# Performance work log

Measured on AMD Instinct MI355X. Metric: run time of the kernel, lower is better.

## Reference

```python
import jax, jax.numpy as jnp
import numpy as np

N, C1, C2 = 1024, 384, 128
H, SQK, SV, PQK, PV, OUT = 12, 16, 16, 4, 8, 384
EPS = 1e-8
DOUT = H*SV + 3*H*PV + H*PV + H*C2  # 2112


def setup_inputs():
    key = jax.random.key(0)
    ks = jax.random.split(key, 10)
    inputs_1d = jax.random.normal(ks[0], (N, C1), jnp.float32)
    inputs_2d = jax.random.normal(ks[1], (N, N, C2), jnp.float32)
    mask = jnp.ones((N, 1), jnp.float32)
    # random valid rotations from unit quaternions
    quat = jax.random.normal(ks[2], (N, 4), jnp.float32)
    quat = quat / jnp.linalg.norm(quat, axis=-1, keepdims=True)
    w, x, y, z = quat[:, 0], quat[:, 1], quat[:, 2], quat[:, 3]
    rot = jnp.stack([
        jnp.stack([1 - 2*(y*y + z*z), 2*(x*y - w*z), 2*(x*z + w*y)], -1),
        jnp.stack([2*(x*y + w*z), 1 - 2*(x*x + z*z), 2*(y*z - w*x)], -1),
        jnp.stack([2*(x*z - w*y), 2*(y*z + w*x), 1 - 2*(x*x + y*y)], -1)], -2)
    trans = 10.0 * jax.random.normal(ks[3], (N, 3), jnp.float32)
    s1 = 1.0 / np.sqrt(C1)
    wq = jax.random.normal(ks[4], (C1, H*SQK), jnp.float32) * s1
    bq = jnp.zeros((H*SQK,), jnp.float32)
    wkv = jax.random.normal(ks[5], (C1, H*(SQK + SV)), jnp.float32) * s1
    bkv = jnp.zeros((H*(SQK + SV),), jnp.float32)
    wqp = jax.random.normal(ks[6], (C1, H*3*PQK), jnp.float32) * s1
    bqp = jnp.zeros((H*3*PQK,), jnp.float32)
    wkvp = jax.random.normal(ks[7], (C1, H*3*(PQK + PV)), jnp.float32) * s1
    bkvp = jnp.zeros((H*3*(PQK + PV),), jnp.float32)
    w2d = jax.random.normal(ks[8], (C2, H), jnp.float32) / np.sqrt(C2)
    b2d = jnp.zeros((H,), jnp.float32)
    tpw = jnp.full((H,), np.log(np.e - 1.0), jnp.float32)  # softplus(tpw)=1 at init
    wo = jax.random.normal(ks[9], (DOUT, OUT), jnp.float32) / np.sqrt(DOUT)
    bo = jnp.zeros((OUT,), jnp.float32)
    return dict(inputs_1d=inputs_1d, inputs_2d=inputs_2d, mask=mask, rot=rot, trans=trans,
                wq=wq, bq=bq, wkv=wkv, bkv=bkv, wqp=wqp, bqp=bqp, wkvp=wkvp, bkvp=bkvp,
                w2d=w2d, b2d=b2d, tpw=tpw, wo=wo, bo=bo)


def _ipa(inputs_1d, inputs_2d, mask, rot, trans, wq, bq, wkv, bkv, wqp, bqp,
         wkvp, bkvp, w2d, b2d, tpw, wo, bo):
    n = inputs_1d.shape[0]
    # scalar q/k/v
    q_scalar = (inputs_1d @ wq + bq).reshape(n, H, SQK)
    kv_scalar = (inputs_1d @ wkv + bkv).reshape(n, H, SQK + SV)
    k_scalar, v_scalar = kv_scalar[..., :SQK], kv_scalar[..., SQK:]
    # point q/k/v: local frame -> global frame, x_g = R x_l + t
    q_pl = (inputs_1d @ wqp + bqp).reshape(n, 3, H*PQK)
    q_pg = jnp.einsum('nac,nck->nak', rot, q_pl) + trans[:, :, None]
    q_pt = q_pg.reshape(n, 3, H, PQK).transpose(1, 2, 0, 3)        # (3,H,N,PQK)
    kv_pl = (inputs_1d @ wkvp + bkvp).reshape(n, 3, H*(PQK + PV))
    kv_pg = jnp.einsum('nac,nck->nak', rot, kv_pl) + trans[:, :, None]
    kv_pt = kv_pg.reshape(n, 3, H, PQK + PV).transpose(1, 2, 0, 3)  # (3,H,N,PQK+PV)
    k_pt, v_pt = kv_pt[..., :PQK], kv_pt[..., PQK:]
    # logit weights (3 logit terms)
    scalar_w = np.sqrt(1.0 / (3.0 * SQK))
    point_w = np.sqrt(1.0 / (3.0 * PQK * 9.0 / 2.0)) * jax.nn.softplus(tpw)  # (H,)
    # squared-distance term, expanded to avoid a (3,H,N,N,P) intermediate
    sq = jnp.sum(q_pt * q_pt, axis=(0, 3))                         # (H,N)
    sk = jnp.sum(k_pt * k_pt, axis=(0, 3))                         # (H,N)
    qk = jnp.einsum('chnp,chmp->hnm', q_pt, k_pt)
    dist2 = sq[:, :, None] + sk[:, None, :] - 2.0 * qk             # (H,N,N)
    attn_qk_point = -0.5 * point_w[:, None, None] * dist2
    attn_qk_scalar = jnp.einsum('nhs,mhs->hnm', scalar_w * q_scalar, k_scalar)
    att2d = jnp.transpose(inputs_2d @ w2d + b2d, (2, 0, 1))        # (H,N,N)
    logits = attn_qk_scalar + attn_qk_point + np.sqrt(1.0 / 3.0) * att2d
    mask_2d = mask * jnp.swapaxes(mask, -1, -2)                    # (N,N)
    logits = logits - 1e5 * (1.0 - mask_2d)
    attn = jax.nn.softmax(logits, axis=-1)                         # (H,N,N)
    # aggregate scalar, point and pair outputs with the same weights
    res_scalar = jnp.einsum('hnm,mhs->nhs', attn, v_scalar).reshape(n, H*SV)
    res_pg = jnp.einsum('hnm,chmp->cnhp', attn, v_pt).reshape(3, n, H*PV)
    res_pl = jnp.einsum('nca,cnk->ank', rot, res_pg - trans.T[:, :, None])  # R^T(g-t)
    pt_norm = jnp.sqrt(EPS + jnp.sum(res_pl * res_pl, axis=0))     # (N,H*PV)
    res_2d = jnp.einsum('hnm,nmc->nhc', attn, inputs_2d).reshape(n, H*C2)
    final = jnp.concatenate([res_scalar, res_pl[0], res_pl[1], res_pl[2], pt_norm, res_2d], axis=-1)
    return final @ wo + bo


def reference(inputs_1d, inputs_2d, mask, rot, trans, wq, bq, wkv, bkv, wqp, bqp,
              wkvp, bkvp, w2d, b2d, tpw, wo, bo):
    return _ipa(inputs_1d, inputs_2d, mask, rot, trans, wq, bq, wkv, bkv, wqp, bqp,
                wkvp, bkvp, w2d, b2d, tpw, wo, bo)
```

## Files before the change

### kernel.cpp

```cpp
#include <hip/hip_runtime.h>
#include <math.h>

#define NN_ 1024
#define DOUT_ 2112
#define NOUT_ 384

using bf16x8_t = __attribute__((ext_vector_type(8))) short;
using f32x4_t  = __attribute__((ext_vector_type(4))) float;

__global__ __launch_bounds__(256) void k_gemm1(
    const float* __restrict__ in1,
    const float* __restrict__ wq, const float* __restrict__ bq,
    const float* __restrict__ wkv, const float* __restrict__ bkv,
    const float* __restrict__ wqp, const float* __restrict__ bqp,
    const float* __restrict__ wkvp, const float* __restrict__ bkvp,
    float* __restrict__ yraw)
{
    __shared__ float a_l[64 * 36];
    __shared__ float b_l[32 * 68];
    const int t = threadIdx.x;
    const int m0 = blockIdx.x * 64, j0 = blockIdx.y * 64;
    const int tx = t & 15, ty = t >> 4;
    float acc[4][4] = {};
    for (int k0 = 0; k0 < 384; k0 += 32) {
        #pragma unroll
        for (int e = 0; e < 2; ++e) {
            int idx = t + 256 * e;
            int r = idx >> 3, c4 = (idx & 7) * 4;
            *(float4*)&a_l[r * 36 + c4] = *(const float4*)&in1[(size_t)(m0 + r) * 384 + k0 + c4];
        }
        #pragma unroll
        for (int e = 0; e < 2; ++e) {
            int idx = t + 256 * e;
            int r = idx >> 4, c4 = (idx & 15) * 4;
            int j = j0 + c4;
            const float* w; int ncol, jj;
            if (j < 192)      { w = wq;   ncol = 192; jj = j; }
            else if (j < 576) { w = wkv;  ncol = 384; jj = j - 192; }
            else if (j < 720) { w = wqp;  ncol = 144; jj = j - 576; }
            else              { w = wkvp; ncol = 432; jj = j - 720; }
            *(float4*)&b_l[r * 68 + c4] = *(const float4*)&w[(size_t)(k0 + r) * ncol + jj];
        }
        __syncthreads();
        #pragma unroll 8
        for (int k = 0; k < 32; ++k) {
            float4 bv = *(const float4*)&b_l[k * 68 + tx * 4];
            #pragma unroll
            for (int i = 0; i < 4; ++i) {
                float av = a_l[(ty * 4 + i) * 36 + k];
                acc[i][0] += av * bv.x; acc[i][1] += av * bv.y;
                acc[i][2] += av * bv.z; acc[i][3] += av * bv.w;
            }
        }
        __syncthreads();
    }
    int j = j0 + tx * 4;
    float4 bias;
    {
        const float* b; int jj;
        if (j < 192)      { b = bq;   jj = j; }
        else if (j < 576) { b = bkv;  jj = j - 192; }
        else if (j < 720) { b = bqp;  jj = j - 576; }
        else              { b = bkvp; jj = j - 720; }
        bias = *(const float4*)&b[jj];
    }
    #pragma unroll
    for (int i = 0; i < 4; ++i) {
        float4 o;
        o.x = acc[i][0] + bias.x; o.y = acc[i][1] + bias.y;
        o.z = acc[i][2] + bias.z; o.w = acc[i][3] + bias.w;
        *(float4*)&yraw[(size_t)(m0 + ty * 4 + i) * 1152 + j] = o;
    }
}

__global__ __launch_bounds__(256) void k_rot(
    const float* __restrict__ yraw, const float* __restrict__ rotm, const float* __restrict__ trans,
    float* __restrict__ qp_arr, float* __restrict__ kpackT4, float* __restrict__ vpack,
    float* __restrict__ sq_arr, float* __restrict__ skT)
{
    __shared__ float rt_l[4][12];
    const int t = threadIdx.x;
    const int n0 = blockIdx.x * 4;
    if (t < 48) {
        int n_ = t / 12, i = t % 12;
        rt_l[n_][i] = (i < 9) ? rotm[(n0 + n_) * 9 + i] : trans[(n0 + n_) * 3 + (i - 9)];
    }
    __syncthreads();
    const int n_ = t >> 6, l = t & 63;
    const int n = n0 + n_;
    const float* y = yraw + (size_t)n * 1152;
    const float* R = rt_l[n_];
    #pragma unroll
    for (int jj = 0; jj < 9; ++jj) {
        int o = l + 64 * jj;
        if (o < 144) {
            int a = o / 48, kk = o % 48;
            float v = R[9 + a] + R[a*3+0] * y[576 + kk] + R[a*3+1] * y[576 + 48 + kk] + R[a*3+2] * y[576 + 96 + kk];
            qp_arr[(size_t)n * 144 + o] = v;
        } else if (o < 288) {
            int o2 = o - 144;
            int a = o2 / 48, r2 = o2 % 48;
            int kk = (r2 >> 2) * 12 + (r2 & 3);
            float v = R[9 + a] + R[a*3+0] * y[720 + kk] + R[a*3+1] * y[720 + 144 + kk] + R[a*3+2] * y[720 + 288 + kk];
            int j = 192 + o2;
            kpackT4[(size_t)(j >> 2) * 4096 + 4 * n + (j & 3)] = v;
        } else {
            int o3 = o - 288;
            int a = o3 / 96, r2 = o3 % 96;
            int kk = (r2 >> 3) * 12 + 4 + (r2 & 7);
            float v = R[9 + a] + R[a*3+0] * y[720 + kk] + R[a*3+1] * y[720 + 144 + kk] + R[a*3+2] * y[720 + 288 + kk];
            vpack[(size_t)n * 480 + 192 + o3] = v;
        }
    }
    #pragma unroll
    for (int jj = 0; jj < 3; ++jj) {
        int o = l + 64 * jj;
        int h = o >> 4, r2 = o & 15;
        kpackT4[(size_t)(o >> 2) * 4096 + 4 * n + (o & 3)] = y[192 + h * 32 + r2];
        vpack[(size_t)n * 480 + o] = y[192 + h * 32 + 16 + r2];
    }
    if (l < 24) {
        int which = l / 12, h = l % 12;
        int base = (which == 0) ? 576 : 720;
        int stride = (which == 0) ? 48 : 144;
        float s = 0.f;
        #pragma unroll
        for (int a = 0; a < 3; ++a) {
            #pragma unroll
            for (int p = 0; p < 4; ++p) {
                int kk = (which == 0) ? (h * 4 + p) : (h * 12 + p);
                float v = R[9 + a] + R[a*3+0] * y[base + kk] + R[a*3+1] * y[base + stride + kk] + R[a*3+2] * y[base + 2 * stride + kk];
                s += v * v;
            }
        }
        if (which == 0) sq_arr[(size_t)n * 12 + h] = s;
        else            skT[(size_t)h * 1024 + n] = s;
    }
}

__global__ __launch_bounds__(256) void k_attn8(
    const float* __restrict__ x2d, const float* __restrict__ mask,
    const float* __restrict__ w2d, const float* __restrict__ b2d, const float* __restrict__ tpw,
    const float* __restrict__ yraw, const float* __restrict__ qp_arr,
    const float* __restrict__ kpackT4, const float* __restrict__ vpack,
    const float* __restrict__ sq_arr, const float* __restrict__ skT,
    const float* __restrict__ rotm, const float* __restrict__ trans,
    float* __restrict__ fin)
{
    __shared__ unsigned short x_lT[128][72];
    __shared__ unsigned short tlb[16][72];
    __shared__ unsigned short w2bT[16][132];
    __shared__ float at2_l[64][13];
    __shared__ float qs_l[192], qp_l[144];
    __shared__ float sq_l[12], pw_l[12], b2_l[12];
    __shared__ float rmax_l[12], rsum_l[16], alph_l[16];
    __shared__ float rt_l[12];
    __shared__ float pg_l[288];

    const int t = threadIdx.x;
    const int n = blockIdx.x;

    const int wv = t >> 6, ln = t & 63;
    const int mmS = ln & 15, oS = ln >> 4;
    const int m3 = t & 63, hg = t >> 6;
    const int rowB = (ln >> 4) * 4;
    const int jF = 2 * t;
    const int hF = (jF < 192) ? (jF >> 4) : (((jF - 192) % 96) >> 3);

    f32x4_t accM[2] = {{0.f, 0.f, 0.f, 0.f}, {0.f, 0.f, 0.f, 0.f}};
    float accF0 = 0.f, accF1 = 0.f;
    float4 xpf[8];

    for (int i = t; i < 2112; i += 256) {
        int h = i / 132, c = i % 132;
        unsigned short v = 0;
        if (h < 12 && c < 128) v = (unsigned short)((__float_as_uint(w2d[c * 12 + h]) + 0x8000u) >> 16);
        w2bT[h][c] = v;
    }
    if (t < 192) qs_l[t] = yraw[(size_t)n * 1152 + t];
    if (t < 144) qp_l[t] = qp_arr[(size_t)n * 144 + t];
    if (t < 12) {
        sq_l[t] = sq_arr[(size_t)n * 12 + t];
        pw_l[t] = 0.13608276348795434f * log1pf(__expf(tpw[t]));
        b2_l[t] = b2d[t];
        rmax_l[t] = -3.0e38f;
        rt_l[t] = (t < 9) ? rotm[n * 9 + t] : trans[n * 3 + (t - 9)];
    }
    if (t < 16) { rsum_l[t] = 0.f; alph_l[t] = 1.0f; }
    const float maskn = mask[n];

    {
        const float* xr = x2d + ((size_t)n * NN_ + wv * 16 + mmS) * 128 + oS * 8;
        #pragma unroll
        for (int kk = 0; kk < 4; ++kk) {
            xpf[2 * kk]     = *(const float4*)&xr[kk * 32];
            xpf[2 * kk + 1] = *(const float4*)&xr[kk * 32 + 4];
        }
    }
    __syncthreads();

    for (int mt = 0; mt < 16; ++mt) {
        const int m0 = mt * 64;
        {
            bf16x8_t afr[4];
            #pragma unroll
            for (int kk = 0; kk < 4; ++kk) {
                unsigned short e0 = (unsigned short)((__float_as_uint(xpf[2*kk].x)   + 0x8000u) >> 16);
                unsigned short e1 = (unsigned short)((__float_as_uint(xpf[2*kk].y)   + 0x8000u) >> 16);
                unsigned short e2 = (unsigned short)((__float_as_uint(xpf[2*kk].z)   + 0x8000u) >> 16);
                unsigned short e3 = (unsigned short)((__float_as_uint(xpf[2*kk].w)   + 0x8000u) >> 16);
                unsigned short e4 = (unsigned short)((__float_as_uint(xpf[2*kk+1].x) + 0x8000u) >> 16);
                unsigned short e5 = (unsigned short)((__float_as_uint(xpf[2*kk+1].y) + 0x8000u) >> 16);
                unsigned short e6 = (unsigned short)((__float_as_uint(xpf[2*kk+1].z) + 0x8000u) >> 16);
                unsigned short e7 = (unsigned short)((__float_as_uint(xpf[2*kk+1].w) + 0x8000u) >> 16);
                afr[kk][0] = (short)e0; afr[kk][1] = (short)e1; afr[kk][2] = (short)e2; afr[kk][3] = (short)e3;
                afr[kk][4] = (short)e4; afr[kk][5] = (short)e5; afr[kk][6] = (short)e6; afr[kk][7] = (short)e7;
                const int c0 = kk * 32 + oS * 8;
                const int m = wv * 16 + mmS;
                x_lT[c0 + 0][m] = e0; x_lT[c0 + 1][m] = e1;
                x_lT[c0 + 2][m] = e2; x_lT[c0 + 3][m] = e3;
                x_lT[c0 + 4][m] = e4; x_lT[c0 + 5][m] = e5;
                x_lT[c0 + 6][m] = e6; x_lT[c0 + 7][m] = e7;
            }
            f32x4_t aA = {0.f, 0.f, 0.f, 0.f};
            #pragma unroll
            for (int kk = 0; kk < 4; ++kk) {
                bf16x8_t bfW = *(const bf16x8_t*)&w2bT[ln & 15][kk * 32 + (ln >> 4) * 8];
                aA = __builtin_amdgcn_mfma_f32_16x16x32_bf16(afr[kk], bfW, aA, 0, 0, 0);
            }
            const int hC = ln & 15;
            if (hC < 12) {
                #pragma unroll
                for (int r = 0; r < 4; ++r)
                    at2_l[wv * 16 + (ln >> 4) * 4 + r][hC] = aA[r];
            }
        }
        __syncthreads();

        {
            int m1 = (mt + 1 == 16) ? 0 : (m0 + 64);
            const float* xr = x2d + ((size_t)n * NN_ + m1 + wv * 16 + mmS) * 128 + oS * 8;
            #pragma unroll
            for (int kk = 0; kk < 4; ++kk) {
                xpf[2 * kk]     = *(const float4*)&xr[kk * 32];
                xpf[2 * kk + 1] = *(const float4*)&xr[kk * 32 + 4];
            }
        }
        {
            const int mg = m0 + m3;
            const float* kb = kpackT4 + 4 * (size_t)mg;
            const float mko = 100000.0f * (1.0f - maskn * mask[mg]);
            #pragma unroll
            for (int e = 0; e < 3; ++e) {
                const int h = hg * 3 + e;
                float4 k0 = *(const float4*)&kb[(size_t)(h * 4 + 0) * 4096];
                float4 k1 = *(const float4*)&kb[(size_t)(h * 4 + 1) * 4096];
                float4 k2 = *(const float4*)&kb[(size_t)(h * 4 + 2) * 4096];
                float4 k3 = *(const float4*)&kb[(size_t)(h * 4 + 3) * 4096];
                float4 p0 = *(const float4*)&kb[(size_t)(48 + h) * 4096];
                float4 p1 = *(const float4*)&kb[(size_t)(60 + h) * 4096];
                float4 p2 = *(const float4*)&kb[(size_t)(72 + h) * 4096];
                float skm = skT[(size_t)h * 1024 + mg];
                const float4* qsn = (const float4*)&qs_l[h * 16];
                float dqs = qsn[0].x*k0.x + qsn[0].y*k0.y + qsn[0].z*k0.z + qsn[0].w*k0.w
                          + qsn[1].x*k1.x + qsn[1].y*k1.y + qsn[1].z*k1.z + qsn[1].w*k1.w
                          + qsn[2].x*k2.x + qsn[2].y*k2.y + qsn[2].z*k2.z + qsn[2].w*k2.w
                          + qsn[3].x*k3.x + qsn[3].y*k3.y + qsn[3].z*k3.z + qsn[3].w*k3.w;
                float4 qA = *(const float4*)&qp_l[h * 4];
                float4 qB = *(const float4*)&qp_l[48 + h * 4];
                float4 qC = *(const float4*)&qp_l[96 + h * 4];
                float qk = qA.x*p0.x + qA.y*p0.y + qA.z*p0.z + qA.w*p0.w
                         + qB.x*p1.x + qB.y*p1.y + qB.z*p1.z + qB.w*p1.w
                         + qC.x*p2.x + qC.y*p2.y + qC.z*p2.z + qC.w*p2.w;
                float pwh = pw_l[h];
                float lg = 0.14433756729740643f * dqs
                         + pwh * qk - 0.5f * pwh * (sq_l[h] + skm)
                         + 0.57735026918962576f * (at2_l[m3][h] + b2_l[h])
                         - mko;
                float tm = lg;
                tm = fmaxf(tm, __shfl_xor(tm, 1));
                tm = fmaxf(tm, __shfl_xor(tm, 2));
                tm = fmaxf(tm, __shfl_xor(tm, 4));
                tm = fmaxf(tm, __shfl_xor(tm, 8));
                tm = fmaxf(tm, __shfl_xor(tm, 16));
                tm = fmaxf(tm, __shfl_xor(tm, 32));
                float om = rmax_l[h];
                float nm = fmaxf(om, tm);
                float p = __expf(lg - nm);
                tlb[h][m3] = (unsigned short)((__float_as_uint(p) + 0x8000u) >> 16);
                float ps = p;
                ps += __shfl_xor(ps, 1);
                ps += __shfl_xor(ps, 2);
                ps += __shfl_xor(ps, 4);
                ps += __shfl_xor(ps, 8);
                ps += __shfl_xor(ps, 16);
                ps += __shfl_xor(ps, 32);
                if (m3 == 0) {
                    float al = __expf(om - nm);
                    rmax_l[h] = nm;
                    alph_l[h] = al;
                    rsum_l[h] = rsum_l[h] * al + ps;
                }
            }
        }
        __syncthreads();

        {
            f32x4_t av = { alph_l[rowB], alph_l[rowB + 1], alph_l[rowB + 2], alph_l[rowB + 3] };
            accM[0] *= av;
            accM[1] *= av;
            bf16x8_t pA0 = *(const bf16x8_t*)&tlb[ln & 15][(ln >> 4) * 8];
            bf16x8_t pA1 = *(const bf16x8_t*)&tlb[ln & 15][32 + (ln >> 4) * 8];
            #pragma unroll
            for (int nt = 0; nt < 2; ++nt) {
                int c = wv * 32 + nt * 16 + (ln & 15);
                bf16x8_t xB0 = *(const bf16x8_t*)&x_lT[c][(ln >> 4) * 8];
                bf16x8_t xB1 = *(const bf16x8_t*)&x_lT[c][32 + (ln >> 4) * 8];
                accM[nt] = __builtin_amdgcn_mfma_f32_16x16x32_bf16(pA0, xB0, accM[nt], 0, 0, 0);
                accM[nt] = __builtin_amdgcn_mfma_f32_16x16x32_bf16(pA1, xB1, accM[nt], 0, 0, 0);
            }
        }
        if (t < 240) {
            float alf = alph_l[hF];
            accF0 *= alf; accF1 *= alf;
            const float* vb = vpack + (size_t)m0 * 480 + jF;
            #pragma unroll 4
            for (int mm = 0; mm < 64; mm += 4) {
                ushort4 pu = *(const ushort4*)&tlb[hF][mm];
                float pa0 = __uint_as_float((unsigned)pu.x << 16);
                float pa1 = __uint_as_float((unsigned)pu.y << 16);
                float pa2 = __uint_as_float((unsigned)pu.z << 16);
                float pa3 = __uint_as_float((unsigned)pu.w << 16);
                float2 v0 = *(const float2*)&vb[(size_t)(mm + 0) * 480];
                float2 v1 = *(const float2*)&vb[(size_t)(mm + 1) * 480];
                float2 v2 = *(const float2*)&vb[(size_t)(mm + 2) * 480];
                float2 v3 = *(const float2*)&vb[(size_t)(mm + 3) * 480];
                accF0 += pa0 * v0.x + pa1 * v1.x + pa2 * v2.x + pa3 * v3.x;
                accF1 += pa0 * v0.y + pa1 * v1.y + pa2 * v2.y + pa3 * v3.y;
            }
        }
        __syncthreads();
    }

    #pragma unroll
    for (int nt = 0; nt < 2; ++nt) {
        #pragma unroll
        for (int r = 0; r < 4; ++r) {
            int row = rowB + r;
            if (row < 12) {
                int c = wv * 32 + nt * 16 + (ln & 15);
                fin[(size_t)n * DOUT_ + 576 + (size_t)row * 128 + c] = accM[nt][r] / rsum_l[row];
            }
        }
    }
    if (t < 240) {
        float inv = 1.f / rsum_l[hF];
        float vA = accF0 * inv, vB = accF1 * inv;
        if (jF < 192) {
            fin[(size_t)n * DOUT_ + jF]     = vA;
            fin[(size_t)n * DOUT_ + jF + 1] = vB;
        } else {
            pg_l[jF - 192] = vA;
            pg_l[jF - 191] = vB;
        }
    }
    __syncthreads();
    if (t < 96) {
        const int k = t;
        float c0 = pg_l[k]       - rt_l[9];
        float c1 = pg_l[96 + k]  - rt_l[10];
        float c2 = pg_l[192 + k] - rt_l[11];
        float r0 = rt_l[0] * c0 + rt_l[3] * c1 + rt_l[6] * c2;
        float r1 = rt_l[1] * c0 + rt_l[4] * c1 + rt_l[7] * c2;
        float r2 = rt_l[2] * c0 + rt_l[5] * c1 + rt_l[8] * c2;
        size_t base = (size_t)n * DOUT_;
        fin[base + 192 + k] = r0;
        fin[base + 288 + k] = r1;
        fin[base + 384 + k] = r2;
        fin[base + 480 + k] = sqrtf(1e-8f + r0 * r0 + r1 * r1 + r2 * r2);
    }
}

__global__ __launch_bounds__(256) void k_out(
    const float* __restrict__ fin, const float* __restrict__ wo,
    float* __restrict__ pout)
{
    __shared__ float a_l[64 * 52];
    __shared__ float b_l[48 * 68];
    const int t = threadIdx.x;
    const int m0 = blockIdx.x * 64, n0 = blockIdx.y * 64, kc = blockIdx.z;
    const int tx = t & 15, ty = t >> 4;
    float acc[4][4] = {};
    for (int k0 = kc * 528; k0 < kc * 528 + 528; k0 += 48) {
        #pragma unroll
        for (int e = 0; e < 3; ++e) {
            int idx = t + 256 * e;
            int r = idx / 12, c4 = (idx % 12) * 4;
            *(float4*)&a_l[r * 52 + c4] = *(const float4*)&fin[(size_t)(m0 + r) * DOUT_ + k0 + c4];
        }
        #pragma unroll
        for (int e = 0; e < 3; ++e) {
            int idx = t + 256 * e;
            int r = idx >> 4, c4 = (idx & 15) * 4;
            *(float4*)&b_l[r * 68 + c4] = *(const float4*)&wo[(size_t)(k0 + r) * 384 + n0 + c4];
        }
        __syncthreads();
        #pragma unroll 4
        for (int k = 0; k < 48; ++k) {
            float4 bv = *(const float4*)&b_l[k * 68 + tx * 4];
            #pragma unroll
            for (int i = 0; i < 4; ++i) {
                float av = a_l[(ty * 4 + i) * 52 + k];
                acc[i][0] += av * bv.x; acc[i][1] += av * bv.y;
                acc[i][2] += av * bv.z; acc[i][3] += av * bv.w;
            }
        }
        __syncthreads();
    }
    float* pr = pout + (size_t)kc * 393216;
    #pragma unroll
    for (int i = 0; i < 4; ++i) {
        float4 o;
        o.x = acc[i][0]; o.y = acc[i][1]; o.z = acc[i][2]; o.w = acc[i][3];
        *(float4*)&pr[(size_t)(m0 + ty * 4 + i) * 384 + n0 + tx * 4] = o;
    }
}

__global__ __launch_bounds__(256) void k_fin(
    const float* __restrict__ pout, const float* __restrict__ bo, float* __restrict__ out)
{
    int idx = blockIdx.x * 256 + threadIdx.x;
    float4 a = *(const float4*)&pout[(size_t)idx * 4];
    float4 b = *(const float4*)&pout[393216 + (size_t)idx * 4];
    float4 c = *(const float4*)&pout[786432 + (size_t)idx * 4];
    float4 d = *(const float4*)&pout[1179648 + (size_t)idx * 4];
    float4 bias = *(const float4*)&bo[(idx % 96) * 4];
    float4 o;
    o.x = a.x + b.x + c.x + d.x + bias.x;
    o.y = a.y + b.y + c.y + d.y + bias.y;
    o.z = a.z + b.z + c.z + d.z + bias.z;
    o.w = a.w + b.w + c.w + d.w + bias.w;
    *(float4*)&out[(size_t)idx * 4] = o;
}

extern "C" void kernel_launch(void* const* d_in, const int* in_sizes, int n_in,
                              void* d_out, int out_size, void* d_ws, size_t ws_size,
                              hipStream_t stream) {
    const float* in1   = (const float*)d_in[0];
    const float* x2d   = (const float*)d_in[1];
    const float* mask  = (const float*)d_in[2];
    const float* rotm  = (const float*)d_in[3];
    const float* trans = (const float*)d_in[4];
    const float* wq    = (const float*)d_in[5];
    const float* bq    = (const float*)d_in[6];
    const float* wkv   = (const float*)d_in[7];
    const float* bkv   = (const float*)d_in[8];
    const float* wqp   = (const float*)d_in[9];
    const float* bqp   = (const float*)d_in[10];
    const float* wkvp  = (const float*)d_in[11];
    const float* bkvp  = (const float*)d_in[12];
    const float* w2d   = (const float*)d_in[13];
    const float* b2d   = (const float*)d_in[14];
    const float* tpw   = (const float*)d_in[15];
    const float* wo    = (const float*)d_in[16];
    const float* bo    = (const float*)d_in[17];
    float* out = (float*)d_out;

    float* ws = (float*)d_ws;
    float* yraw    = ws;
    float* qp_arr  = yraw + 1179648;
    float* kpackT4 = qp_arr + 147456;
    float* vpack   = kpackT4 + 360448;
    float* sq_arr  = vpack + 491520;
    float* fin     = sq_arr + 12288;
    float* pout    = fin + 2162688;
    float* skT     = pout + 1572864;

    hipLaunchKernelGGL(k_gemm1, dim3(16, 18), dim3(256), 0, stream,
        in1, wq, bq, wkv, bkv, wqp, bqp, wkvp, bkvp, yraw);
    hipLaunchKernelGGL(k_rot, dim3(256), dim3(256), 0, stream,
        yraw, rotm, trans, qp_arr, kpackT4, vpack, sq_arr, skT);
    hipLaunchKernelGGL(k_attn8, dim3(1024), dim3(256), 0, stream,
        x2d, mask, w2d, b2d, tpw, yraw, qp_arr, kpackT4, vpack, sq_arr, skT, rotm, trans, fin);
    hipLaunchKernelGGL(k_out, dim3(16, 6, 4), dim3(256), 0, stream, fin, wo, pout);
    hipLaunchKernelGGL(k_fin, dim3(384), dim3(256), 0, stream, pout, bo, out);
}
```

Measured before the change: 382.5 us.

## Aggregate scalar/point values with fp16 MFMA using transposed fp16 value layout

```diff
diff --git a/kernel.cpp b/kernel.cpp
--- a/kernel.cpp
+++ b/kernel.cpp
@@ -5,8 +5,8 @@
 #define DOUT_ 2112
 #define NOUT_ 384
 
-using bf16x8_t = __attribute__((ext_vector_type(8))) short;
-using f32x4_t  = __attribute__((ext_vector_type(4))) float;
+using f16x8_t = __attribute__((ext_vector_type(8))) _Float16;
+using f32x4_t = __attribute__((ext_vector_type(4))) float;
 
 __global__ __launch_bounds__(256) void k_gemm1(
     const float* __restrict__ in1,
@@ -75,7 +75,7 @@
 
 __global__ __launch_bounds__(256) void k_rot(
     const float* __restrict__ yraw, const float* __restrict__ rotm, const float* __restrict__ trans,
-    float* __restrict__ qp_arr, float* __restrict__ kpackT4, float* __restrict__ vpack,
+    float* __restrict__ qp_arr, float* __restrict__ kpackT4, _Float16* __restrict__ vT,
     float* __restrict__ sq_arr, float* __restrict__ skT)
 {
     __shared__ float rt_l[4][12];
@@ -109,7 +109,7 @@
             int a = o3 / 96, r2 = o3 % 96;
             int kk = (r2 >> 3) * 12 + 4 + (r2 & 7);
             float v = R[9 + a] + R[a*3+0] * y[720 + kk] + R[a*3+1] * y[720 + 144 + kk] + R[a*3+2] * y[720 + 288 + kk];
-            vpack[(size_t)n * 480 + 192 + o3] = v;
+            vT[(size_t)(192 + o3) * 1024 + n] = (_Float16)v;
         }
     }
     #pragma unroll
@@ -117,8 +117,9 @@
         int o = l + 64 * jj;
         int h = o >> 4, r2 = o & 15;
         kpackT4[(size_t)(o >> 2) * 4096 + 4 * n + (o & 3)] = y[192 + h * 32 + r2];
-        vpack[(size_t)n * 480 + o] = y[192 + h * 32 + 16 + r2];
-    }
+        vT[(size_t)o * 1024 + n] = (_Float16)y[192 + h * 32 + 16 + r2];
+    }
+    if (l < 32) vT[(size_t)(480 + l) * 1024 + n] = (_Float16)0.f;
     if (l < 24) {
         int which = l / 12, h = l % 12;
         int base = (which == 0) ? 576 : 720;
@@ -138,18 +139,18 @@
     }
 }
 
-__global__ __launch_bounds__(256) void k_attn8(
+__global__ __launch_bounds__(256) void k_attn9(
     const float* __restrict__ x2d, const float* __restrict__ mask,
     const float* __restrict__ w2d, const float* __restrict__ b2d, const float* __restrict__ tpw,
     const float* __restrict__ yraw, const float* __restrict__ qp_arr,
-    const float* __restrict__ kpackT4, const float* __restrict__ vpack,
+    const float* __restrict__ kpackT4, const _Float16* __restrict__ vT,
     const float* __restrict__ sq_arr, const float* __restrict__ skT,
     const float* __restrict__ rotm, const float* __restrict__ trans,
     float* __restrict__ fin)
 {
-    __shared__ unsigned short x_lT[128][72];
-    __shared__ unsigned short tlb[16][72];
-    __shared__ unsigned short w2bT[16][132];
+    __shared__ _Float16 x_lT[128][72];
+    __shared__ _Float16 tlb[16][72];
+    __shared__ _Float16 w2bT[16][136];
     __shared__ float at2_l[64][13];
     __shared__ float qs_l[192], qp_l[144];
     __shared__ float sq_l[12], pw_l[12], b2_l[12];
@@ -164,19 +165,18 @@
     const int mmS = ln & 15, oS = ln >> 4;
     const int m3 = t & 63, hg = t >> 6;
     const int rowB = (ln >> 4) * 4;
-    const int jF = 2 * t;
-    const int hF = (jF < 192) ? (jF >> 4) : (((jF - 192) % 96) >> 3);
-
-    f32x4_t accM[2] = {{0.f, 0.f, 0.f, 0.f}, {0.f, 0.f, 0.f, 0.f}};
-    float accF0 = 0.f, accF1 = 0.f;
-    float4 xpf[8];
-
-    for (int i = t; i < 2112; i += 256) {
-        int h = i / 132, c = i % 132;
-        unsigned short v = 0;
-        if (h < 12 && c < 128) v = (unsigned short)((__float_as_uint(w2d[c * 12 + h]) + 0x8000u) >> 16);
-        w2bT[h][c] = v;
-    }
+
+    f32x4_t accM[2] = {{0.f,0.f,0.f,0.f},{0.f,0.f,0.f,0.f}};
+    f32x4_t accF[8];
+    #pragma unroll
+    for (int jt = 0; jt < 8; ++jt) accF[jt] = (f32x4_t){0.f,0.f,0.f,0.f};
+    f16x8_t afr[4];
+
+    for (int i = t; i < 2176; i += 256) {
+        int h = i / 136, c = i % 136;
+        w2bT[h][c] = (h < 12 && c < 128) ? (_Float16)w2d[c * 12 + h] : (_Float16)0.f;
+    }
+    tlb[12 + (t >> 6)][t & 63] = (_Float16)0.f;
     if (t < 192) qs_l[t] = yraw[(size_t)n * 1152 + t];
     if (t < 144) qp_l[t] = qp_arr[(size_t)n * 144 + t];
     if (t < 12) {
@@ -193,8 +193,12 @@
         const float* xr = x2d + ((size_t)n * NN_ + wv * 16 + mmS) * 128 + oS * 8;
         #pragma unroll
         for (int kk = 0; kk < 4; ++kk) {
-            xpf[2 * kk]     = *(const float4*)&xr[kk * 32];
-            xpf[2 * kk + 1] = *(const float4*)&xr[kk * 32 + 4];
+            float4 a = *(const float4*)&xr[kk * 32];
+            float4 b = *(const float4*)&xr[kk * 32 + 4];
+            f16x8_t f;
+            f[0]=(_Float16)a.x; f[1]=(_Float16)a.y; f[2]=(_Float16)a.z; f[3]=(_Float16)a.w;
+            f[4]=(_Float16)b.x; f[5]=(_Float16)b.y; f[6]=(_Float16)b.z; f[7]=(_Float16)b.w;
+            afr[kk] = f;
         }
     }
     __syncthreads();
@@ -202,31 +206,18 @@
     for (int mt = 0; mt < 16; ++mt) {
         const int m0 = mt * 64;
         {
-            bf16x8_t afr[4];
+            const int m = wv * 16 + mmS;
             #pragma unroll
             for (int kk = 0; kk < 4; ++kk) {
-                unsigned short e0 = (unsigned short)((__float_as_uint(xpf[2*kk].x)   + 0x8000u) >> 16);
-                unsigned short e1 = (unsigned short)((__float_as_uint(xpf[2*kk].y)   + 0x8000u) >> 16);
-                unsigned short e2 = (unsigned short)((__float_as_uint(xpf[2*kk].z)   + 0x8000u) >> 16);
-                unsigned short e3 = (unsigned short)((__float_as_uint(xpf[2*kk].w)   + 0x8000u) >> 16);
-                unsigned short e4 = (unsigned short)((__float_as_uint(xpf[2*kk+1].x) + 0x8000u) >> 16);
-                unsigned short e5 = (unsigned short)((__float_as_uint(xpf[2*kk+1].y) + 0x8000u) >> 16);
-                unsigned short e6 = (unsigned short)((__float_as_uint(xpf[2*kk+1].z) + 0x8000u) >> 16);
-                unsigned short e7 = (unsigned short)((__float_as_uint(xpf[2*kk+1].w) + 0x8000u) >> 16);
-                afr[kk][0] = (short)e0; afr[kk][1] = (short)e1; afr[kk][2] = (short)e2; afr[kk][3] = (short)e3;
-                afr[kk][4] = (short)e4; afr[kk][5] = (short)e5; afr[kk][6] = (short)e6; afr[kk][7] = (short)e7;
                 const int c0 = kk * 32 + oS * 8;
-                const int m = wv * 16 + mmS;
-                x_lT[c0 + 0][m] = e0; x_lT[c0 + 1][m] = e1;
-                x_lT[c0 + 2][m] = e2; x_lT[c0 + 3][m] = e3;
-                x_lT[c0 + 4][m] = e4; x_lT[c0 + 5][m] = e5;
-                x_lT[c0 + 6][m] = e6; x_lT[c0 + 7][m] = e7;
+                #pragma unroll
+                for (int i = 0; i < 8; ++i) x_lT[c0 + i][m] = afr[kk][i];
             }
             f32x4_t aA = {0.f, 0.f, 0.f, 0.f};
             #pragma unroll
             for (int kk = 0; kk < 4; ++kk) {
-                bf16x8_t bfW = *(const bf16x8_t*)&w2bT[ln & 15][kk * 32 + (ln >> 4) * 8];
-                aA = __builtin_amdgcn_mfma_f32_16x16x32_bf16(afr[kk], bfW, aA, 0, 0, 0);
+                f16x8_t bfW = *(const f16x8_t*)&w2bT[ln & 15][kk * 32 + (ln >> 4) * 8];
+                aA = __builtin_amdgcn_mfma_f32_16x16x32_f16(afr[kk], bfW, aA, 0, 0, 0);
             }
             const int hC = ln & 15;
             if (hC < 12) {
@@ -242,8 +233,12 @@
             const float* xr = x2d + ((size_t)n * NN_ + m1 + wv * 16 + mmS) * 128 + oS * 8;
             #pragma unroll
             for (int kk = 0; kk < 4; ++kk) {
-                xpf[2 * kk]     = *(const float4*)&xr[kk * 32];
-                xpf[2 * kk + 1] = *(const float4*)&xr[kk * 32 + 4];
+                float4 a = *(const float4*)&xr[kk * 32];
+                float4 b = *(const float4*)&xr[kk * 32 + 4];
+                f16x8_t f;
+                f[0]=(_Float16)a.x; f[1]=(_Float16)a.y; f[2]=(_Float16)a.z; f[3]=(_Float16)a.w;
+                f[4]=(_Float16)b.x; f[5]=(_Float16)b.y; f[6]=(_Float16)b.z; f[7]=(_Float16)b.w;
+                afr[kk] = f;
             }
         }
         {
@@ -287,7 +282,7 @@
                 float om = rmax_l[h];
                 float nm = fmaxf(om, tm);
                 float p = __expf(lg - nm);
-                tlb[h][m3] = (unsigned short)((__float_as_uint(p) + 0x8000u) >> 16);
+                tlb[h][m3] = (_Float16)p;
                 float ps = p;
                 ps += __shfl_xor(ps, 1);
                 ps += __shfl_xor(ps, 2);
@@ -309,34 +304,26 @@
             f32x4_t av = { alph_l[rowB], alph_l[rowB + 1], alph_l[rowB + 2], alph_l[rowB + 3] };
             accM[0] *= av;
             accM[1] *= av;
-            bf16x8_t pA0 = *(const bf16x8_t*)&tlb[ln & 15][(ln >> 4) * 8];
-            bf16x8_t pA1 = *(const bf16x8_t*)&tlb[ln & 15][32 + (ln >> 4) * 8];
+            #pragma unroll
+            for (int jt = 0; jt < 8; ++jt) accF[jt] *= av;
+            f16x8_t pA0 = *(const f16x8_t*)&tlb[ln & 15][(ln >> 4) * 8];
+            f16x8_t pA1 = *(const f16x8_t*)&tlb[ln & 15][32 + (ln >> 4) * 8];
             #pragma unroll
             for (int nt = 0; nt < 2; ++nt) {
                 int c = wv * 32 + nt * 16 + (ln & 15);
-                bf16x8_t xB0 = *(const bf16x8_t*)&x_lT[c][(ln >> 4) * 8];
-                bf16x8_t xB1 = *(const bf16x8_t*)&x_lT[c][32 + (ln >> 4) * 8];
-                accM[nt] = __builtin_amdgcn_mfma_f32_16x16x32_bf16(pA0, xB0, accM[nt], 0, 0, 0);
-                accM[nt] = __builtin_amdgcn_mfma_f32_16x16x32_bf16(pA1, xB1, accM[nt], 0, 0, 0);
-            }
-        }
-        if (t < 240) {
-            float alf = alph_l[hF];
-            accF0 *= alf; accF1 *= alf;
-            const float* vb = vpack + (size_t)m0 * 480 + jF;
-            #pragma unroll 4
-            for (int mm = 0; mm < 64; mm += 4) {
-                ushort4 pu = *(const ushort4*)&tlb[hF][mm];
-                float pa0 = __uint_as_float((unsigned)pu.x << 16);
-                float pa1 = __uint_as_float((unsigned)pu.y << 16);
-                float pa2 = __uint_as_float((unsigned)pu.z << 16);
-                float pa3 = __uint_as_float((unsigned)pu.w << 16);
-                float2 v0 = *(const float2*)&vb[(size_t)(mm + 0) * 480];
-                float2 v1 = *(const float2*)&vb[(size_t)(mm + 1) * 480];
-                float2 v2 = *(const float2*)&vb[(size_t)(mm + 2) * 480];
-                float2 v3 = *(const float2*)&vb[(size_t)(mm + 3) * 480];
-                accF0 += pa0 * v0.x + pa1 * v1.x + pa2 * v2.x + pa3 * v3.x;
-                accF1 += pa0 * v0.y + pa1 * v1.y + pa2 * v2.y + pa3 * v3.y;
+                f16x8_t xB0 = *(const f16x8_t*)&x_lT[c][(ln >> 4) * 8];
+                f16x8_t xB1 = *(const f16x8_t*)&x_lT[c][32 + (ln >> 4) * 8];
+                accM[nt] = __builtin_amdgcn_mfma_f32_16x16x32_f16(pA0, xB0, accM[nt], 0, 0, 0);
+                accM[nt] = __builtin_amdgcn_mfma_f32_16x16x32_f16(pA1, xB1, accM[nt], 0, 0, 0);
+            }
+            const _Float16* vb = vT + (size_t)m0;
+            #pragma unroll
+            for (int jt = 0; jt < 8; ++jt) {
+                int j = (wv * 8 + jt) * 16 + (ln & 15);
+                f16x8_t vB0 = *(const f16x8_t*)&vb[(size_t)j * 1024 + (ln >> 4) * 8];
+                f16x8_t vB1 = *(const f16x8_t*)&vb[(size_t)j * 1024 + 32 + (ln >> 4) * 8];
+                accF[jt] = __builtin_amdgcn_mfma_f32_16x16x32_f16(pA0, vB0, accF[jt], 0, 0, 0);
+                accF[jt] = __builtin_amdgcn_mfma_f32_16x16x32_f16(pA1, vB1, accF[jt], 0, 0, 0);
             }
         }
         __syncthreads();
@@ -353,15 +340,16 @@
             }
         }
     }
-    if (t < 240) {
-        float inv = 1.f / rsum_l[hF];
-        float vA = accF0 * inv, vB = accF1 * inv;
-        if (jF < 192) {
-            fin[(size_t)n * DOUT_ + jF]     = vA;
-            fin[(size_t)n * DOUT_ + jF + 1] = vB;
-        } else {
-            pg_l[jF - 192] = vA;
-            pg_l[jF - 191] = vB;
+    #pragma unroll
+    for (int jt = 0; jt < 8; ++jt) {
+        int j = (wv * 8 + jt) * 16 + (ln & 15);
+        if (j < 480) {
+            int hj = (j < 192) ? (j >> 4) : (((j - 192) % 96) >> 3);
+            if (hj >= rowB && hj < rowB + 4) {
+                float val = accF[jt][hj - rowB] / rsum_l[hj];
+                if (j < 192) fin[(size_t)n * DOUT_ + j] = val;
+                else         pg_l[j - 192] = val;
+            }
         }
     }
     __syncthreads();
@@ -470,18 +458,19 @@
     float* yraw    = ws;
     float* qp_arr  = yraw + 1179648;
     float* kpackT4 = qp_arr + 147456;
-    float* vpack   = kpackT4 + 360448;
-    float* sq_arr  = vpack + 491520;
+    float* vT_f    = kpackT4 + 360448;
+    float* sq_arr  = vT_f + 262144;
     float* fin     = sq_arr + 12288;
     float* pout    = fin + 2162688;
     float* skT     = pout + 1572864;
+    _Float16* vT = (_Float16*)vT_f;
 
     hipLaunchKernelGGL(k_gemm1, dim3(16, 18), dim3(256), 0, stream,
         in1, wq, bq, wkv, bkv, wqp, bqp, wkvp, bkvp, yraw);
     hipLaunchKernelGGL(k_rot, dim3(256), dim3(256), 0, stream,
-        yraw, rotm, trans, qp_arr, kpackT4, vpack, sq_arr, skT);
-    hipLaunchKernelGGL(k_attn8, dim3(1024), dim3(256), 0, stream,
-        x2d, mask, w2d, b2d, tpw, yraw, qp_arr, kpackT4, vpack, sq_arr, skT, rotm, trans, fin);
+        yraw, rotm, trans, qp_arr, kpackT4, vT, sq_arr, skT);
+    hipLaunchKernelGGL(k_attn9, dim3(1024), dim3(256), 0, stream,
+        x2d, mask, w2d, b2d, tpw, yraw, qp_arr, kpackT4, vT, sq_arr, skT, rotm, trans, fin);
     hipLaunchKernelGGL(k_out, dim3(16, 6, 4), dim3(256), 0, stream, fin, wo, pout);
     hipLaunchKernelGGL(k_fin, dim3(384), dim3(256), 0, stream, pout, bo, out);
 }
```

Result: faster. 360.5 us (-5.7%).
